# Performance work log

Hardware: AMD Instinct MI355X
Metric: run time of the kernel (lower is better)

Reference implementation:

```python
import jax, jax.numpy as jnp
import numpy as np

D_MODEL = 1024
N_HEADS = 16
HEAD_DIM = D_MODEL // N_HEADS
BATCH = 4
SEQ = 2048


def setup_inputs() -> dict:
    key = jax.random.key(0)
    k_x, k_wqkv, k_bqkv, k_wo, k_bo = jax.random.split(key, 5)
    x = jax.random.normal(k_x, (BATCH, SEQ, D_MODEL), dtype=jnp.float32)
    # causal mask: True = masked (upper triangle, excluding diagonal)
    mask = jnp.triu(jnp.ones((SEQ, SEQ), dtype=bool), k=1)
    lim = 1.0 / np.sqrt(D_MODEL)
    w_qkv = jax.random.uniform(k_wqkv, (D_MODEL, 3 * D_MODEL), jnp.float32, -lim, lim)
    b_qkv = jax.random.uniform(k_bqkv, (3 * D_MODEL,), jnp.float32, -lim, lim)
    w_out = jax.random.uniform(k_wo, (D_MODEL, D_MODEL), jnp.float32, -lim, lim)
    b_out = jax.random.uniform(k_bo, (D_MODEL,), jnp.float32, -lim, lim)
    return {"x": x, "mask": mask, "w_qkv": w_qkv, "b_qkv": b_qkv,
            "w_out": w_out, "b_out": b_out}


def reference(x, mask, w_qkv, b_qkv, w_out, b_out):
    b, s, _ = x.shape
    scale = HEAD_DIM ** -0.5
    qkv = x @ w_qkv + b_qkv                          # [b, s, 3*d]
    qkv = qkv.reshape(b, s, 3, N_HEADS, HEAD_DIM)
    qkv = jnp.transpose(qkv, (2, 0, 3, 1, 4))        # [3, b, h, s, hd]
    q, k, v = qkv[0], qkv[1], qkv[2]
    attn = jnp.einsum('bhqd,bhkd->bhqk', q, k) * scale
    attn = jnp.where(mask, -jnp.inf, attn)
    attn = jax.nn.softmax(attn, axis=-1)
    out = jnp.einsum('bhqk,bhkd->bhqd', attn, v)     # [b, h, s, hd]
    out = jnp.transpose(out, (0, 2, 1, 3)).reshape(b, s, D_MODEL)
    return out @ w_out + b_out
```

## Files before the change

### kernel.cpp

```cpp
#include <hip/hip_runtime.h>
#include <stdint.h>

typedef unsigned short u16;
typedef __attribute__((ext_vector_type(8))) short short8;
typedef __attribute__((ext_vector_type(4))) float f32x4;
typedef __attribute__((ext_vector_type(16))) float f32x16;

#define DEV static __device__ __forceinline__

#define QSCALE 0.18033688011112042f

DEV float fast_exp2(float x) { return __builtin_amdgcn_exp2f(x); }

DEV float bf2f(u16 u) { union { uint32_t i; float f; } x; x.i = ((uint32_t)u) << 16; return x.f; }
DEV u16 f2bf(float f) {
  union { float f; uint32_t i; } x; x.f = f;
  uint32_t r = x.i + 0x7FFFu + ((x.i >> 16) & 1u);
  return (u16)(r >> 16);
}
DEV uint32_t pk_bf16(float lo, float hi) {
  uint32_t r;
  asm("v_cvt_pk_bf16_f32 %0, %1, %2" : "=v"(r) : "v"(lo), "v"(hi));
  return r;
}

DEV void async_copy16(void* lds_dst, const void* gsrc) {
  typedef __attribute__((address_space(1))) void* gp_t;
  typedef __attribute__((address_space(3))) void* lp_t;
  __builtin_amdgcn_global_load_lds((gp_t)(uintptr_t)gsrc,
                                   (lp_t)(uint32_t)(uintptr_t)lds_dst, 16, 0, 0);
}

DEV void gemm_bt_core(const u16* __restrict__ A, const u16* __restrict__ Bt, int K,
                      int m0, int n0, uint8_t* As, uint8_t* Bs,
                      f32x4 (&acc)[4][4], int wave, int lane, int wm, int wn) {
#pragma unroll
  for (int mt = 0; mt < 4; ++mt)
#pragma unroll
    for (int nt = 0; nt < 4; ++nt)
      acc[mt][nt] = (f32x4){0.f, 0.f, 0.f, 0.f};

  for (int k0 = 0; k0 < K; k0 += 64) {
    __syncthreads();
#pragma unroll
    for (int i = 0; i < 4; ++i) {
      int cb = wave * 256 + i * 64;
      int c  = cb + lane;
      int r  = c >> 3;
      int ks = (c & 7) ^ (r & 7);
      async_copy16(As + cb * 16 + lane * 16, A  + (size_t)(m0 + r) * K + k0 + ks * 8);
      async_copy16(Bs + cb * 16 + lane * 16, Bt + (size_t)(n0 + r) * K + k0 + ks * 8);
    }
    __syncthreads();

    short8 af[2][4], bf_[2][4];
#pragma unroll
    for (int kk = 0; kk < 2; ++kk)
#pragma unroll
      for (int t = 0; t < 4; ++t) {
        int ra = wm + t * 16 + (lane & 15);
        af[kk][t]  = *(const short8*)(As + ra * 128 + (((kk * 4 + (lane >> 4)) ^ (ra & 7)) << 4));
        int rb = wn + t * 16 + (lane & 15);
        bf_[kk][t] = *(const short8*)(Bs + rb * 128 + (((kk * 4 + (lane >> 4)) ^ (rb & 7)) << 4));
      }
#pragma unroll
    for (int kk = 0; kk < 2; ++kk)
#pragma unroll
      for (int mt = 0; mt < 4; ++mt)
#pragma unroll
        for (int nt = 0; nt < 4; ++nt)
          acc[mt][nt] = __builtin_amdgcn_mfma_f32_16x16x32_bf16(af[kk][mt], bf_[kk][nt],
                                                                acc[mt][nt], 0, 0, 0);
  }
}

__global__ __launch_bounds__(256, 2) void k_gemm_qkv(
    const u16* __restrict__ X, const u16* __restrict__ WT, const float* __restrict__ bias,
    u16* __restrict__ Q, u16* __restrict__ Kv, u16* __restrict__ Vt) {
  __shared__ __attribute__((aligned(16))) uint8_t As[16384];
  __shared__ __attribute__((aligned(16))) uint8_t Bs[16384];
  const int lane = threadIdx.x & 63, wave = threadIdx.x >> 6;
  const int wm = (wave >> 1) * 64, wn = (wave & 1) * 64;
  const int m0 = blockIdx.x * 128, n0 = blockIdx.y * 128;
  f32x4 acc[4][4];
  gemm_bt_core(X, WT, 1024, m0, n0, As, Bs, acc, wave, lane, wm, wn);
#pragma unroll
  for (int nt = 0; nt < 4; ++nt) {
    int n = n0 + wn + nt * 16 + (lane & 15);
    float bv = bias[n];
    int which = n >> 10, h = (n >> 6) & 15, hd = n & 63;
    if (which == 2) {
#pragma unroll
      for (int mt = 0; mt < 4; ++mt) {
        int m = m0 + wm + mt * 16 + (lane >> 4) * 4;
        int b = m >> 11, s = m & 2047;
        u16 tmp[4];
#pragma unroll
        for (int rg = 0; rg < 4; ++rg) tmp[rg] = f2bf(acc[mt][nt][rg] + bv);
        *(uint64_t*)(Vt + ((size_t)(b * 16 + h) * 64 + hd) * 2048 + s) = *(const uint64_t*)tmp;
      }
    } else {
      u16* base = (which == 0) ? Q : Kv;
      const float mul = (which == 0) ? QSCALE : 1.0f;
#pragma unroll
      for (int mt = 0; mt < 4; ++mt)
#pragma unroll
        for (int rg = 0; rg < 4; ++rg) {
          int m = m0 + wm + mt * 16 + (lane >> 4) * 4 + rg;
          int b = m >> 11, s = m & 2047;
          base[((size_t)(b * 16 + h) * 2048 + s) * 64 + hd] = f2bf((acc[mt][nt][rg] + bv) * mul);
        }
    }
  }
}

__global__ __launch_bounds__(256, 2) void k_gemm_out(
    const u16* __restrict__ A, const u16* __restrict__ WT, const float* __restrict__ bias,
    float* __restrict__ Out) {
  __shared__ __attribute__((aligned(16))) uint8_t As[16384];
  __shared__ __attribute__((aligned(16))) uint8_t Bs[16384];
  const int lane = threadIdx.x & 63, wave = threadIdx.x >> 6;
  const int wm = (wave >> 1) * 64, wn = (wave & 1) * 64;
  const int m0 = blockIdx.x * 128, n0 = blockIdx.y * 128;
  f32x4 acc[4][4];
  gemm_bt_core(A, WT, 1024, m0, n0, As, Bs, acc, wave, lane, wm, wn);
#pragma unroll
  for (int nt = 0; nt < 4; ++nt) {
    int n = n0 + wn + nt * 16 + (lane & 15);
    float bv = bias[n];
#pragma unroll
    for (int mt = 0; mt < 4; ++mt)
#pragma unroll
      for (int rg = 0; rg < 4; ++rg) {
        int m = m0 + wm + mt * 16 + (lane >> 4) * 4 + rg;
        Out[(size_t)m * 1024 + n] = acc[mt][nt][rg] + bv;
      }
  }
}

__global__ __launch_bounds__(256) void k_cvt_x(const float* __restrict__ src,
                                               u16* __restrict__ dst, int n8) {
  int i = blockIdx.x * 256 + threadIdx.x;
  if (i >= n8) return;
  float4 a = *(const float4*)(src + (size_t)i * 8);
  float4 b = *(const float4*)(src + (size_t)i * 8 + 4);
  u16 tmp[8] = {f2bf(a.x), f2bf(a.y), f2bf(a.z), f2bf(a.w),
                f2bf(b.x), f2bf(b.y), f2bf(b.z), f2bf(b.w)};
  *(short8*)(dst + (size_t)i * 8) = *(const short8*)tmp;
}

__global__ __launch_bounds__(256) void k_transpose_f32(
    const float* __restrict__ src, u16* __restrict__ dst, int R, int C) {
  __shared__ u16 tile[64][72];
  const int tr = blockIdx.x * 64, tc = blockIdx.y * 64;
  for (int c = threadIdx.x; c < 1024; c += 256) {
    int r = c >> 4, c4 = (c & 15) * 4;
    float4 v = *(const float4*)(src + (size_t)(tr + r) * C + tc + c4);
    tile[r][c4 + 0] = f2bf(v.x); tile[r][c4 + 1] = f2bf(v.y);
    tile[r][c4 + 2] = f2bf(v.z); tile[r][c4 + 3] = f2bf(v.w);
  }
  __syncthreads();
  for (int c = threadIdx.x; c < 512; c += 256) {
    int oc = c >> 3, r8 = (c & 7) * 8;
    u16 tmp[8];
#pragma unroll
    for (int i = 0; i < 8; ++i) tmp[i] = tile[r8 + i][oc];
    *(short8*)(dst + (size_t)(tc + oc) * R + tr + r8) = *(const short8*)tmp;
  }
}

DEV void stage_tile(const u16* __restrict__ Kg, const u16* __restrict__ Vg,
                    uint8_t* kb, uint8_t* vb, int t, int tid) {
#pragma unroll
  for (int i = 0; i < 2; ++i) {
    int c = i * 256 + tid;
    int r = c >> 3;
    int ks = (c & 7) ^ (r & 7);
    async_copy16(kb + c * 16, Kg + (size_t)(t * 64 + r) * 64 + ks * 8);
    async_copy16(vb + c * 16, Vg + (size_t)r * 2048 + t * 64 + ks * 8);
  }
}

__global__ __launch_bounds__(256, 4) void k_attn(
    const u16* __restrict__ Q, const u16* __restrict__ K,
    const u16* __restrict__ Vt, u16* __restrict__ O) {
  __shared__ __attribute__((aligned(16))) uint8_t kbuf[2][8192];
  __shared__ __attribute__((aligned(16))) uint8_t vbuf[2][8192];
  const int tid = threadIdx.x;
  const int lane = tid & 63;
  const int wave = tid >> 6;
  const int q32 = lane & 31, hv = lane >> 5;
  const float NEG_INF = -__builtin_inff();

  int L = blockIdx.x;
  int j = L >> 3;
  int bh = (L & 7) * 8 + (j >> 4);
  int pair = j & 15;
  const int b = bh >> 4, h = bh & 15;
  const size_t hb = (size_t)bh * (2048 * 64);
  const u16* Qg = Q + hb;
  const u16* Kg = K + hb;
  const u16* Vg = Vt + hb;

  const int s = (wave < 2) ? pair : (31 - pair);
  const int nt_blk = 32 - pair;
  const int my_nt = s + 1;
  const int qbase = s * 64 + (wave & 1) * 32;
  const int qg = qbase + q32;

  short8 qf[4];
#pragma unroll
  for (int dblk = 0; dblk < 4; ++dblk)
    qf[dblk] = *(const short8*)(Qg + (size_t)qg * 64 + dblk * 16 + hv * 8);

  f32x16 oacc[2] = {};
  float mrun = NEG_INF, lrun = 0.f;

  stage_tile(Kg, Vg, kbuf[0], vbuf[0], 0, tid);
  __syncthreads();

#pragma unroll 1
  for (int t = 0; t < nt_blk; ++t) {
    const int cur = t & 1;
    if (t + 1 < nt_blk) stage_tile(Kg, Vg, kbuf[cur ^ 1], vbuf[cur ^ 1], t + 1, tid);

    if (t < my_nt) {
      const uint8_t* kb = kbuf[cur];
      const uint8_t* vb = vbuf[cur];

      f32x16 sa0 = {}, sa1 = {};
      __builtin_amdgcn_s_setprio(1);
#pragma unroll
      for (int dblk = 0; dblk < 4; ++dblk) {
        short8 kf0 = *(const short8*)(kb + q32 * 128 + (((dblk * 2 + hv) ^ (q32 & 7)) << 4));
        short8 kf1 = *(const short8*)(kb + (32 + q32) * 128 + (((dblk * 2 + hv) ^ (q32 & 7)) << 4));
        sa0 = __builtin_amdgcn_mfma_f32_32x32x16_bf16(kf0, qf[dblk], sa0, 0, 0, 0);
        sa1 = __builtin_amdgcn_mfma_f32_32x32x16_bf16(kf1, qf[dblk], sa1, 0, 0, 0);
      }
      __builtin_amdgcn_s_setprio(0);

      float sv[32];
#pragma unroll
      for (int r = 0; r < 16; ++r) { sv[r] = sa0[r]; sv[16 + r] = sa1[r]; }
      if (t == s) {
#pragma unroll
        for (int r = 0; r < 16; ++r) {
          int kl = (r & 3) + 8 * (r >> 2) + 4 * hv;
          if (t * 64 + kl > qg)      sv[r]      = NEG_INF;
          if (t * 64 + 32 + kl > qg) sv[16 + r] = NEG_INF;
        }
      }

      float mloc = fmaxf(sv[0], sv[1]);
#pragma unroll
      for (int r = 2; r < 32; ++r) mloc = fmaxf(mloc, sv[r]);
      float mtile = fmaxf(mloc, __shfl_xor(mloc, 32, 64));
      if (!__all(mtile <= mrun + 8.f)) {
        float mnew = fmaxf(mrun, mtile);
        float corr = fast_exp2(mrun - mnew);
        mrun = mnew;
        lrun *= corr;
#pragma unroll
        for (int r = 0; r < 16; ++r) { oacc[0][r] *= corr; oacc[1][r] *= corr; }
      }
      float ls = 0.f;
#pragma unroll
      for (int r = 0; r < 32; ++r) { sv[r] = fast_exp2(sv[r] - mrun); ls += sv[r]; }
      ls += __shfl_xor(ls, 32, 64);
      lrun += ls;

      __builtin_amdgcn_s_setprio(1);
#pragma unroll
      for (int ksub = 0; ksub < 2; ++ksub) {
#pragma unroll
        for (int kb2 = 0; kb2 < 2; ++kb2) {
          const int rb = ksub * 16 + kb2 * 8;
          uint32_t pA = pk_bf16(sv[rb + 0], sv[rb + 1]);
          uint32_t pB = pk_bf16(sv[rb + 2], sv[rb + 3]);
          uint32_t pC = pk_bf16(sv[rb + 4], sv[rb + 5]);
          uint32_t pD = pk_bf16(sv[rb + 6], sv[rb + 7]);
          uint32_t X = hv ? pA : pC;
          uint32_t Y = hv ? pB : pD;
          uint32_t sX = (uint32_t)__shfl_xor((int)X, 32, 64);
          uint32_t sY = (uint32_t)__shfl_xor((int)Y, 32, 64);
          union { uint32_t u[4]; short8 s8; } pu;
          pu.u[0] = hv ? sX : pA;
          pu.u[1] = hv ? sY : pB;
          pu.u[2] = hv ? pC : sX;
          pu.u[3] = hv ? pD : sY;
          const int kblk = ksub * 2 + kb2;
          short8 vf0 = *(const short8*)(vb + q32 * 128 + (((kblk * 2 + hv) ^ (q32 & 7)) << 4));
          short8 vf1 = *(const short8*)(vb + (32 + q32) * 128 + (((kblk * 2 + hv) ^ (q32 & 7)) << 4));
          oacc[0] = __builtin_amdgcn_mfma_f32_32x32x16_bf16(vf0, pu.s8, oacc[0], 0, 0, 0);
          oacc[1] = __builtin_amdgcn_mfma_f32_32x32x16_bf16(vf1, pu.s8, oacc[1], 0, 0, 0);
        }
      }
      __builtin_amdgcn_s_setprio(0);
    }

    __syncthreads();
  }

  float rl = 1.0f / lrun;
  u16* orow = O + ((size_t)(b * 2048 + qg)) * 1024 + h * 64;
#pragma unroll
  for (int dt = 0; dt < 2; ++dt)
#pragma unroll
    for (int g = 0; g < 4; ++g) {
      int dbase = dt * 32 + 8 * g + 4 * hv;
      u16 tmp[4];
#pragma unroll
      for (int j2 = 0; j2 < 4; ++j2) tmp[j2] = f2bf(oacc[dt][4 * g + j2] * rl);
      *(uint64_t*)(orow + dbase) = *(const uint64_t*)tmp;
    }
}

extern "C" void kernel_launch(void* const* d_in, const int* in_sizes, int n_in,
                              void* d_out, int out_size, void* d_ws, size_t ws_size,
                              hipStream_t stream) {
  const float* x     = (const float*)d_in[0];
  const float* w_qkv = (const float*)d_in[2];
  const float* b_qkv = (const float*)d_in[3];
  const float* w_out = (const float*)d_in[4];
  const float* b_out = (const float*)d_in[5];
  float* out = (float*)d_out;
  uint8_t* ws = (uint8_t*)d_ws;

  u16* wqkvT = (u16*)(ws);
  u16* woutT = (u16*)(ws +  6291456);
  u16* Xb    = (u16*)(ws +  8388608);
  u16* Qb    = (u16*)(ws + 25165824);
  u16* Kb    = (u16*)(ws + 41943040);
  u16* Vtb   = (u16*)(ws + 58720256);
  u16* AO    = Xb;

  k_cvt_x<<<dim3(4096), 256, 0, stream>>>(x, Xb, 1048576);
  k_transpose_f32<<<dim3(16, 48), 256, 0, stream>>>(w_qkv, wqkvT, 1024, 3072);
  k_transpose_f32<<<dim3(16, 16), 256, 0, stream>>>(w_out, woutT, 1024, 1024);
  k_gemm_qkv<<<dim3(64, 24), 256, 0, stream>>>(Xb, wqkvT, b_qkv, Qb, Kb, Vtb);
  k_attn<<<dim3(1024), 256, 0, stream>>>(Qb, Kb, Vtb, AO);
  k_gemm_out<<<dim3(64, 8), 256, 0, stream>>>(AO, woutT, b_out, out);
}
```

Baseline: 158.6 us.

## Drop LDS staging in attention; read K/V fragments directly from global memory

Removes the shared-memory double-buffered async K/V staging and the per-tile block barrier. Each wave now loads its MFMA K and V fragments straight from global memory, relying on L1/L2 caching. Query rows are reassigned at 32-row granularity with a mirrored pairing, so each wave runs its own causal tile count without waiting for other waves. Each wave now fetches the same K/V tiles on its own, which raises global/L2 traffic and exposes load latency that the LDS prefetch used to hide.

```diff
diff --git a/kernel.cpp b/kernel.cpp
--- a/kernel.cpp
+++ b/kernel.cpp
@@ -169,43 +169,27 @@
   }
 }
 
-DEV void stage_tile(const u16* __restrict__ Kg, const u16* __restrict__ Vg,
-                    uint8_t* kb, uint8_t* vb, int t, int tid) {
-#pragma unroll
-  for (int i = 0; i < 2; ++i) {
-    int c = i * 256 + tid;
-    int r = c >> 3;
-    int ks = (c & 7) ^ (r & 7);
-    async_copy16(kb + c * 16, Kg + (size_t)(t * 64 + r) * 64 + ks * 8);
-    async_copy16(vb + c * 16, Vg + (size_t)r * 2048 + t * 64 + ks * 8);
-  }
-}
-
 __global__ __launch_bounds__(256, 4) void k_attn(
     const u16* __restrict__ Q, const u16* __restrict__ K,
     const u16* __restrict__ Vt, u16* __restrict__ O) {
-  __shared__ __attribute__((aligned(16))) uint8_t kbuf[2][8192];
-  __shared__ __attribute__((aligned(16))) uint8_t vbuf[2][8192];
-  const int tid = threadIdx.x;
-  const int lane = tid & 63;
-  const int wave = tid >> 6;
+  const int lane = threadIdx.x & 63;
+  const int wave = threadIdx.x >> 6;
   const int q32 = lane & 31, hv = lane >> 5;
   const float NEG_INF = -__builtin_inff();
 
   int L = blockIdx.x;
-  int j = L >> 3;
-  int bh = (L & 7) * 8 + (j >> 4);
-  int pair = j & 15;
+  int idx = L >> 3;
+  int bh = (L & 7) * 8 + (idx >> 4);
+  int j = idx & 15;
   const int b = bh >> 4, h = bh & 15;
   const size_t hb = (size_t)bh * (2048 * 64);
   const u16* Qg = Q + hb;
   const u16* Kg = K + hb;
   const u16* Vg = Vt + hb;
 
-  const int s = (wave < 2) ? pair : (31 - pair);
-  const int nt_blk = 32 - pair;
-  const int my_nt = s + 1;
-  const int qbase = s * 64 + (wave & 1) * 32;
+  const int s = (wave & 2) ? (62 - 2 * j + (wave & 1)) : (2 * j + (wave & 1));
+  const int nt = (s >> 1) + 1;
+  const int qbase = s * 32;
   const int qg = qbase + q32;
 
   short8 qf[4];
@@ -216,89 +200,79 @@
   f32x16 oacc[2] = {};
   float mrun = NEG_INF, lrun = 0.f;
 
-  stage_tile(Kg, Vg, kbuf[0], vbuf[0], 0, tid);
-  __syncthreads();
-
 #pragma unroll 1
-  for (int t = 0; t < nt_blk; ++t) {
-    const int cur = t & 1;
-    if (t + 1 < nt_blk) stage_tile(Kg, Vg, kbuf[cur ^ 1], vbuf[cur ^ 1], t + 1, tid);
-
-    if (t < my_nt) {
-      const uint8_t* kb = kbuf[cur];
-      const uint8_t* vb = vbuf[cur];
-
-      f32x16 sa0 = {}, sa1 = {};
-      __builtin_amdgcn_s_setprio(1);
-#pragma unroll
-      for (int dblk = 0; dblk < 4; ++dblk) {
-        short8 kf0 = *(const short8*)(kb + q32 * 128 + (((dblk * 2 + hv) ^ (q32 & 7)) << 4));
-        short8 kf1 = *(const short8*)(kb + (32 + q32) * 128 + (((dblk * 2 + hv) ^ (q32 & 7)) << 4));
-        sa0 = __builtin_amdgcn_mfma_f32_32x32x16_bf16(kf0, qf[dblk], sa0, 0, 0, 0);
-        sa1 = __builtin_amdgcn_mfma_f32_32x32x16_bf16(kf1, qf[dblk], sa1, 0, 0, 0);
-      }
-      __builtin_amdgcn_s_setprio(0);
-
-      float sv[32];
-#pragma unroll
-      for (int r = 0; r < 16; ++r) { sv[r] = sa0[r]; sv[16 + r] = sa1[r]; }
-      if (t == s) {
-#pragma unroll
-        for (int r = 0; r < 16; ++r) {
-          int kl = (r & 3) + 8 * (r >> 2) + 4 * hv;
-          if (t * 64 + kl > qg)      sv[r]      = NEG_INF;
-          if (t * 64 + 32 + kl > qg) sv[16 + r] = NEG_INF;
-        }
-      }
-
-      float mloc = fmaxf(sv[0], sv[1]);
-#pragma unroll
-      for (int r = 2; r < 32; ++r) mloc = fmaxf(mloc, sv[r]);
-      float mtile = fmaxf(mloc, __shfl_xor(mloc, 32, 64));
-      if (!__all(mtile <= mrun + 8.f)) {
-        float mnew = fmaxf(mrun, mtile);
-        float corr = fast_exp2(mrun - mnew);
-        mrun = mnew;
-        lrun *= corr;
-#pragma unroll
-        for (int r = 0; r < 16; ++r) { oacc[0][r] *= corr; oacc[1][r] *= corr; }
-      }
-      float ls = 0.f;
-#pragma unroll
-      for (int r = 0; r < 32; ++r) { sv[r] = fast_exp2(sv[r] - mrun); ls += sv[r]; }
-      ls += __shfl_xor(ls, 32, 64);
-      lrun += ls;
-
-      __builtin_amdgcn_s_setprio(1);
-#pragma unroll
-      for (int ksub = 0; ksub < 2; ++ksub) {
-#pragma unroll
-        for (int kb2 = 0; kb2 < 2; ++kb2) {
-          const int rb = ksub * 16 + kb2 * 8;
-          uint32_t pA = pk_bf16(sv[rb + 0], sv[rb + 1]);
-          uint32_t pB = pk_bf16(sv[rb + 2], sv[rb + 3]);
-          uint32_t pC = pk_bf16(sv[rb + 4], sv[rb + 5]);
-          uint32_t pD = pk_bf16(sv[rb + 6], sv[rb + 7]);
-          uint32_t X = hv ? pA : pC;
-          uint32_t Y = hv ? pB : pD;
-          uint32_t sX = (uint32_t)__shfl_xor((int)X, 32, 64);
-          uint32_t sY = (uint32_t)__shfl_xor((int)Y, 32, 64);
-          union { uint32_t u[4]; short8 s8; } pu;
-          pu.u[0] = hv ? sX : pA;
-          pu.u[1] = hv ? sY : pB;
-          pu.u[2] = hv ? pC : sX;
-          pu.u[3] = hv ? pD : sY;
-          const int kblk = ksub * 2 + kb2;
-          short8 vf0 = *(const short8*)(vb + q32 * 128 + (((kblk * 2 + hv) ^ (q32 & 7)) << 4));
-          short8 vf1 = *(const short8*)(vb + (32 + q32) * 128 + (((kblk * 2 + hv) ^ (q32 & 7)) << 4));
-          oacc[0] = __builtin_amdgcn_mfma_f32_32x32x16_bf16(vf0, pu.s8, oacc[0], 0, 0, 0);
-          oacc[1] = __builtin_amdgcn_mfma_f32_32x32x16_bf16(vf1, pu.s8, oacc[1], 0, 0, 0);
-        }
-      }
-      __builtin_amdgcn_s_setprio(0);
-    }
-
-    __syncthreads();
+  for (int t = 0; t < nt; ++t) {
+    const u16* kt  = Kg + (size_t)t * (64 * 64);
+    const u16* vtc = Vg + (size_t)t * 64;
+
+    f32x16 sa0 = {}, sa1 = {};
+    __builtin_amdgcn_s_setprio(1);
+#pragma unroll
+    for (int dblk = 0; dblk < 4; ++dblk) {
+      short8 kf0 = *(const short8*)(kt + (size_t)q32 * 64 + dblk * 16 + hv * 8);
+      short8 kf1 = *(const short8*)(kt + (size_t)(32 + q32) * 64 + dblk * 16 + hv * 8);
+      sa0 = __builtin_amdgcn_mfma_f32_32x32x16_bf16(kf0, qf[dblk], sa0, 0, 0, 0);
+      sa1 = __builtin_amdgcn_mfma_f32_32x32x16_bf16(kf1, qf[dblk], sa1, 0, 0, 0);
+    }
+    __builtin_amdgcn_s_setprio(0);
+
+    float sv[32];
+#pragma unroll
+    for (int r = 0; r < 16; ++r) { sv[r] = sa0[r]; sv[16 + r] = sa1[r]; }
+    if (t * 64 + 63 > qbase) {
+#pragma unroll
+      for (int r = 0; r < 16; ++r) {
+        int kl = (r & 3) + 8 * (r >> 2) + 4 * hv;
+        if (t * 64 + kl > qg)      sv[r]      = NEG_INF;
+        if (t * 64 + 32 + kl > qg) sv[16 + r] = NEG_INF;
+      }
+    }
+
+    float mloc = fmaxf(sv[0], sv[1]);
+#pragma unroll
+    for (int r = 2; r < 32; ++r) mloc = fmaxf(mloc, sv[r]);
+    float mtile = fmaxf(mloc, __shfl_xor(mloc, 32, 64));
+    if (!__all(mtile <= mrun + 8.f)) {
+      float mnew = fmaxf(mrun, mtile);
+      float corr = fast_exp2(mrun - mnew);
+      mrun = mnew;
+      lrun *= corr;
+#pragma unroll
+      for (int r = 0; r < 16; ++r) { oacc[0][r] *= corr; oacc[1][r] *= corr; }
+    }
+    float ls = 0.f;
+#pragma unroll
+    for (int r = 0; r < 32; ++r) { sv[r] = fast_exp2(sv[r] - mrun); ls += sv[r]; }
+    ls += __shfl_xor(ls, 32, 64);
+    lrun += ls;
+
+    __builtin_amdgcn_s_setprio(1);
+#pragma unroll
+    for (int ksub = 0; ksub < 2; ++ksub) {
+#pragma unroll
+      for (int kb2 = 0; kb2 < 2; ++kb2) {
+        const int rb = ksub * 16 + kb2 * 8;
+        uint32_t pA = pk_bf16(sv[rb + 0], sv[rb + 1]);
+        uint32_t pB = pk_bf16(sv[rb + 2], sv[rb + 3]);
+        uint32_t pC = pk_bf16(sv[rb + 4], sv[rb + 5]);
+        uint32_t pD = pk_bf16(sv[rb + 6], sv[rb + 7]);
+        uint32_t X = hv ? pA : pC;
+        uint32_t Y = hv ? pB : pD;
+        uint32_t sX = (uint32_t)__shfl_xor((int)X, 32, 64);
+        uint32_t sY = (uint32_t)__shfl_xor((int)Y, 32, 64);
+        union { uint32_t u[4]; short8 s8; } pu;
+        pu.u[0] = hv ? sX : pA;
+        pu.u[1] = hv ? sY : pB;
+        pu.u[2] = hv ? pC : sX;
+        pu.u[3] = hv ? pD : sY;
+        const int kblk = ksub * 2 + kb2;
+        short8 vf0 = *(const short8*)(vtc + (size_t)q32 * 2048 + (kblk * 2 + hv) * 8);
+        short8 vf1 = *(const short8*)(vtc + (size_t)(32 + q32) * 2048 + (kblk * 2 + hv) * 8);
+        oacc[0] = __builtin_amdgcn_mfma_f32_32x32x16_bf16(vf0, pu.s8, oacc[0], 0, 0, 0);
+        oacc[1] = __builtin_amdgcn_mfma_f32_32x32x16_bf16(vf1, pu.s8, oacc[1], 0, 0, 0);
+      }
+    }
+    __builtin_amdgcn_s_setprio(0);
   }
 
   float rl = 1.0f / lrun;
```

Measured after the change: 221.2 us. +39.5%, slower.
